# Kernel tuning notes

Measured on AMD Instinct MI355X. Metric: run time of the kernel, lower is better.

The kernel has to match this reference:

```python
import jax, jax.numpy as jnp
import numpy as np

NEG_BIAS = 1000000000.0


def setup_inputs() -> dict:
    key = jax.random.key(0)
    k1, k2 = jax.random.split(key)
    B, N, D = 8, 2048, 512
    inputs = jax.random.normal(k1, (B, N, D), dtype=jnp.float32)
    mask = jax.random.randint(k2, (B, N), 0, 2, dtype=jnp.int32)
    return {"inputs": inputs, "mask": mask}


def reference(inputs, mask):
    # inputs: [B, N, D], mask: [B, N]
    d = inputs.shape[-1]
    scale = 1.0 / jnp.sqrt(jnp.asarray(d, dtype=inputs.dtype))
    # e[b,i,j] = <x_i, x_j> / sqrt(d)
    e = jnp.einsum('bid,bjd->bij', inputs, inputs) * scale
    # K.expand_dims(mask) appends axis -1 -> [B, N, 1]; bias broadcasts over keys
    bias = (1.0 - mask.astype(inputs.dtype))[:, :, None] * NEG_BIAS
    e = e - bias
    a = jax.nn.softmax(e, axis=-1)  # [B, N, N]
    v = jnp.einsum('bij,bjd->bid', a, inputs)
    return v
```

## Files before the change

kernel.cpp:

```cpp
#include <hip/hip_runtime.h>

#define Bb 8
#define Nn 2048
#define Dd 512

#define KV 32
#define NT 64
#define SPS 40

#define KVF 64
#define NTF (Nn / KVF)
#define PPF 72

typedef __attribute__((ext_vector_type(8))) short bf8;
typedef __attribute__((ext_vector_type(4))) float f4;
typedef __attribute__((ext_vector_type(16))) float f16v;
struct __align__(16) U8 { unsigned short s[8]; };
struct __align__(8) US4 { unsigned short s[4]; };

__device__ __forceinline__ unsigned short f2bf(float f) {
  union { float f; unsigned u; } v; v.f = f;
  unsigned r = v.u + 0x7fffu + ((v.u >> 16) & 1u);
  return (unsigned short)(r >> 16);
}
__device__ __forceinline__ float bf2f(unsigned short h) {
  union { unsigned u; float f; } v; v.u = ((unsigned)h) << 16; return v.f;
}

__device__ __forceinline__ void gload_lds16(const unsigned short* g, unsigned short* l) {
  __builtin_amdgcn_global_load_lds(
      (const __attribute__((address_space(1))) void*)g,
      (__attribute__((address_space(3))) void*)l, 16, 0, 0);
}

__global__ __launch_bounds__(256)
void build_images(const float* __restrict__ X, unsigned short* __restrict__ W) {
  __shared__ float sT[KV * Dd];
  const int t = blockIdx.x, b = blockIdx.y, tid = threadIdx.x;
  const float* src = X + ((size_t)b * Nn + t * KV) * Dd;
#pragma unroll
  for (int i = 0; i < 16; ++i) {
    int idx = i * 256 + tid;
    *(float4*)(sT + idx * 4) = *(const float4*)(src + idx * 4);
  }
  __syncthreads();
  unsigned short* img = W + ((size_t)(b * NT + t) << 15);
#pragma unroll
  for (int i = 0; i < 8; ++i) {
    int slot = i * 256 + tid;
    int f = slot >> 6, L = slot & 63;
    const float* p = sT + (L & 31) * Dd + f * 16 + (L >> 5) * 8;
    U8 v;
#pragma unroll
    for (int e = 0; e < 8; ++e) v.s[e] = f2bf(p[e]);
    *(U8*)(img + slot * 8) = v;
  }
#pragma unroll
  for (int i = 0; i < 8; ++i) {
    int slot = i * 256 + tid;
    int fv = slot >> 6, L = slot & 63;
    int dcol = (fv >> 1) * 32 + (L & 31);
    int k0 = (fv & 1) * 16 + (L >> 5) * 8;
    U8 v;
#pragma unroll
    for (int e = 0; e < 8; ++e) v.s[e] = f2bf(sT[(k0 + e) * Dd + dcol]);
    *(U8*)(img + 16384 + slot * 8) = v;
  }
}

__global__ __launch_bounds__(512, 1)
void attn32(const unsigned short* __restrict__ W, const int* __restrict__ mask,
            float* __restrict__ out) {
  __shared__ unsigned short sBuf[2][32768];
  __shared__ unsigned short sSx[2 * 16 * 64 * 4];
  __shared__ unsigned short sP[2 * 32 * SPS];

  const int tid  = threadIdx.x;
  const int wave = tid >> 6;
  const int qg = wave >> 2, dq = wave & 3;
  const int lane = tid & 63;
  const int l31 = lane & 31, h = lane >> 5;
  const int rowsh = h * 4;
  const int bid = blockIdx.x;
  const int b = bid & 7;
  const int qb = bid >> 3;
  const int q0 = qb * 64;
  const int bN = b * NT;
  const float scale = 0.044194173824159216f;

  bf8 qf[8];
  {
    const unsigned short* qimg = W + ((size_t)(bN + qb * 2 + qg) << 15);
#pragma unroll
    for (int g = 0; g < 8; ++g)
      qf[g] = *(const bf8*)(qimg + (dq * 8 + g) * 512 + lane * 8);
  }

  float rs16[16];
  {
    int mv = mask[b * Nn + q0 + qg * 32 + l31];
    unsigned mb = (unsigned)(__ballot(mv != 0) & 0xffffffffull);
#pragma unroll
    for (int i = 0; i < 16; ++i) {
      int row = (i & 3) + 8 * (i >> 2) + rowsh;
      rs16[i] = ((mb >> row) & 1u) ? scale : 0.0f;
    }
  }

  bf8 ones;
#pragma unroll
  for (int i = 0; i < 8; ++i) ones[i] = (short)0x3F80;

  f16v o0, o1, o2, o3, lacc;
#pragma unroll
  for (int i = 0; i < 16; ++i) { o0[i] = 0.f; o1[i] = 0.f; o2[i] = 0.f; o3[i] = 0.f; lacc[i] = 0.f; }

  {
    const unsigned short* img0 = W + ((size_t)bN << 15);
#pragma unroll
    for (int i = 0; i < 8; ++i) {
      int chunk = i * 8 + wave;
      gload_lds16(img0 + chunk * 512 + lane * 8, sBuf[0] + chunk * 512);
    }
  }
  __syncthreads();

  int cur = 0;
  for (int t = 0; t < NT; ++t) {
    const unsigned short* sK = sBuf[cur];

    f16v sa, sb;
#pragma unroll
    for (int i = 0; i < 16; ++i) { sa[i] = 0.f; sb[i] = 0.f; }
#pragma unroll
    for (int g2 = 0; g2 < 4; ++g2) {
      bf8 k0 = *(const bf8*)(sK + (dq * 8 + g2 * 2) * 512 + lane * 8);
      bf8 k1 = *(const bf8*)(sK + (dq * 8 + g2 * 2 + 1) * 512 + lane * 8);
      sa = __builtin_amdgcn_mfma_f32_32x32x16_bf16(qf[g2 * 2], k0, sa, 0, 0, 0);
      sb = __builtin_amdgcn_mfma_f32_32x32x16_bf16(qf[g2 * 2 + 1], k1, sb, 0, 0, 0);
    }
#pragma unroll
    for (int i = 0; i < 16; ++i)
      sSx[((qg * 16 + i) * 64 + lane) * 4 + dq] = f2bf(sa[i] + sb[i]);
    __syncthreads();

    if (t + 1 < NT) {
      const unsigned short* gKn = W + ((size_t)(bN + t + 1) << 15);
      unsigned short* nb = sBuf[cur ^ 1];
#pragma unroll
      for (int i = 0; i < 8; ++i) {
        int chunk = i * 8 + wave;
        gload_lds16(gKn + chunk * 512 + lane * 8, nb + chunk * 512);
      }
    }

    unsigned short* Pq = sP + qg * 32 * SPS;
#pragma unroll
    for (int i = 0; i < 16; ++i) {
      US4 v = *(const US4*)(&sSx[((qg * 16 + i) * 64 + lane) * 4]);
      float e = (bf2f(v.s[0]) + bf2f(v.s[1]) + bf2f(v.s[2]) + bf2f(v.s[3])) * rs16[i];
      int row = (i & 3) + 8 * (i >> 2) + rowsh;
      Pq[row * SPS + l31] = f2bf(__expf(e));
    }
    bf8 af0 = *(const bf8*)(Pq + l31 * SPS + h * 8);
    bf8 af1 = *(const bf8*)(Pq + l31 * SPS + 16 + h * 8);

    lacc = __builtin_amdgcn_mfma_f32_32x32x16_bf16(af0, ones, lacc, 0, 0, 0);
    lacc = __builtin_amdgcn_mfma_f32_32x32x16_bf16(af1, ones, lacc, 0, 0, 0);

    const unsigned short* sV = sBuf[cur] + 16384;
    {
      bf8 v0 = *(const bf8*)(sV + ((dq * 4 + 0) * 2) * 512 + lane * 8);
      bf8 v1 = *(const bf8*)(sV + ((dq * 4 + 0) * 2 + 1) * 512 + lane * 8);
      o0 = __builtin_amdgcn_mfma_f32_32x32x16_bf16(af0, v0, o0, 0, 0, 0);
      o0 = __builtin_amdgcn_mfma_f32_32x32x16_bf16(af1, v1, o0, 0, 0, 0);
      v0 = *(const bf8*)(sV + ((dq * 4 + 1) * 2) * 512 + lane * 8);
      v1 = *(const bf8*)(sV + ((dq * 4 + 1) * 2 + 1) * 512 + lane * 8);
      o1 = __builtin_amdgcn_mfma_f32_32x32x16_bf16(af0, v0, o1, 0, 0, 0);
      o1 = __builtin_amdgcn_mfma_f32_32x32x16_bf16(af1, v1, o1, 0, 0, 0);
      v0 = *(const bf8*)(sV + ((dq * 4 + 2) * 2) * 512 + lane * 8);
      v1 = *(const bf8*)(sV + ((dq * 4 + 2) * 2 + 1) * 512 + lane * 8);
      o2 = __builtin_amdgcn_mfma_f32_32x32x16_bf16(af0, v0, o2, 0, 0, 0);
      o2 = __builtin_amdgcn_mfma_f32_32x32x16_bf16(af1, v1, o2, 0, 0, 0);
      v0 = *(const bf8*)(sV + ((dq * 4 + 3) * 2) * 512 + lane * 8);
      v1 = *(const bf8*)(sV + ((dq * 4 + 3) * 2 + 1) * 512 + lane * 8);
      o3 = __builtin_amdgcn_mfma_f32_32x32x16_bf16(af0, v0, o3, 0, 0, 0);
      o3 = __builtin_amdgcn_mfma_f32_32x32x16_bf16(af1, v1, o3, 0, 0, 0);
    }
    __syncthreads();
    cur ^= 1;
  }

#pragma unroll
  for (int i = 0; i < 16; ++i) {
    int row = (i & 3) + 8 * (i >> 2) + rowsh;
    size_t gr = (size_t)b * Nn + q0 + qg * 32 + row;
    float inv = 1.0f / lacc[i];
    out[gr * Dd + dq * 128 + 0 * 32 + l31] = o0[i] * inv;
    out[gr * Dd + dq * 128 + 1 * 32 + l31] = o1[i] * inv;
    out[gr * Dd + dq * 128 + 2 * 32 + l31] = o2[i] * inv;
    out[gr * Dd + dq * 128 + 3 * 32 + l31] = o3[i] * inv;
  }
}

__global__ __launch_bounds__(256, 1)
void attn_fb(const float* __restrict__ Xf, const int* __restrict__ mask,
             float* __restrict__ out) {
  __shared__ unsigned short sKf[KVF * Dd];
  __shared__ unsigned short sVt[Dd * KVF];
  __shared__ unsigned short sPf[4][16 * PPF];

  const int tid  = threadIdx.x;
  const int wave = tid >> 6, lane = tid & 63;
  const int lg = lane >> 4, ll = lane & 15;
  const int b  = blockIdx.y;
  const int q0 = blockIdx.x * 64 + wave * 16;

  bf8 qf[16];
  {
    const size_t qoff = ((size_t)b * Nn + q0 + ll) * Dd;
#pragma unroll
    for (int ch = 0; ch < 16; ++ch) {
      int doff = ch * 32 + lg * 8;
      float4 a = *(const float4*)(Xf + qoff + doff);
      float4 c = *(const float4*)(Xf + qoff + doff + 4);
      bf8 tt;
      tt[0] = (short)f2bf(a.x); tt[1] = (short)f2bf(a.y);
      tt[2] = (short)f2bf(a.z); tt[3] = (short)f2bf(a.w);
      tt[4] = (short)f2bf(c.x); tt[5] = (short)f2bf(c.y);
      tt[6] = (short)f2bf(c.z); tt[7] = (short)f2bf(c.w);
      qf[ch] = tt;
    }
  }
  float bias[4];
#pragma unroll
  for (int r = 0; r < 4; ++r)
    bias[r] = (1.0f - (float)mask[b * Nn + q0 + lg * 4 + r]) * 1e9f;
  float m[4], lsum[4];
  f4 o[32];
#pragma unroll
  for (int r = 0; r < 4; ++r) { m[r] = -1e30f; lsum[r] = 0.0f; }
#pragma unroll
  for (int ct = 0; ct < 32; ++ct) o[ct] = (f4){0.f, 0.f, 0.f, 0.f};
  const float scale = 0.044194173824159216f;

  for (int t = 0; t < NTF; ++t) {
    __syncthreads();
    const size_t base = ((size_t)b * Nn + t * KVF) * Dd;
#pragma unroll
    for (int it = 0; it < 16; ++it) {
      int idx = it * 256 + tid;
      int key = idx >> 6, c = idx & 63;
      const float* sp = Xf + base + key * Dd + c * 8;
      float4 a = *(const float4*)(sp);
      float4 d2 = *(const float4*)(sp + 4);
      U8 v;
      v.s[0] = f2bf(a.x); v.s[1] = f2bf(a.y); v.s[2] = f2bf(a.z); v.s[3] = f2bf(a.w);
      v.s[4] = f2bf(d2.x); v.s[5] = f2bf(d2.y); v.s[6] = f2bf(d2.z); v.s[7] = f2bf(d2.w);
      *(U8*)(sKf + key * 512 + ((c ^ (key & 7)) << 3)) = v;
      int ko = key >> 3, k7 = key & 7;
#pragma unroll
      for (int j = 0; j < 8; ++j) {
        int dd = c * 8 + j;
        sVt[dd * 64 + ((ko ^ j ^ (c & 7)) << 3) + k7] = v.s[j];
      }
    }
    __syncthreads();

    f4 s[4];
#pragma unroll
    for (int cc = 0; cc < 4; ++cc) s[cc] = (f4){0.f, 0.f, 0.f, 0.f};
#pragma unroll
    for (int ch = 0; ch < 16; ++ch)
#pragma unroll
      for (int cc = 0; cc < 4; ++cc) {
        int key = cc * 16 + ll;
        bf8 kf = *(const bf8*)(sKf + key * 512 + (((ch * 4 + lg) ^ (key & 7)) << 3));
        s[cc] = __builtin_amdgcn_mfma_f32_16x16x32_bf16(qf[ch], kf, s[cc], 0, 0, 0);
      }

    float e[4][4];
#pragma unroll
    for (int cc = 0; cc < 4; ++cc)
#pragma unroll
      for (int r = 0; r < 4; ++r) e[cc][r] = s[cc][r] * scale - bias[r];
    float tm[4];
#pragma unroll
    for (int r = 0; r < 4; ++r)
      tm[r] = fmaxf(fmaxf(e[0][r], e[1][r]), fmaxf(e[2][r], e[3][r]));
#pragma unroll
    for (int off = 1; off < 16; off <<= 1)
#pragma unroll
      for (int r = 0; r < 4; ++r) tm[r] = fmaxf(tm[r], __shfl_xor(tm[r], off));
    float mn[4]; bool change = false;
#pragma unroll
    for (int r = 0; r < 4; ++r) { mn[r] = fmaxf(m[r], tm[r]); change = change || (mn[r] > m[r]); }
    if (__any(change)) {
#pragma unroll
      for (int r = 0; r < 4; ++r) {
        float al = __expf(m[r] - mn[r]);
        lsum[r] *= al; m[r] = mn[r];
#pragma unroll
        for (int ct = 0; ct < 32; ++ct) o[ct][r] *= al;
      }
    }
    float ts[4] = {0.f, 0.f, 0.f, 0.f};
    unsigned short pb[4][4];
#pragma unroll
    for (int cc = 0; cc < 4; ++cc)
#pragma unroll
      for (int r = 0; r < 4; ++r) {
        float p = __expf(e[cc][r] - m[r]);
        ts[r] += p; pb[cc][r] = f2bf(p);
      }
#pragma unroll
    for (int off = 1; off < 16; off <<= 1)
#pragma unroll
      for (int r = 0; r < 4; ++r) ts[r] += __shfl_xor(ts[r], off);
#pragma unroll
    for (int r = 0; r < 4; ++r) lsum[r] += ts[r];

    unsigned short* Pw = sPf[wave];
#pragma unroll
    for (int cc = 0; cc < 4; ++cc)
#pragma unroll
      for (int r = 0; r < 4; ++r)
        Pw[(lg * 4 + r) * PPF + cc * 16 + ll] = pb[cc][r];
#pragma unroll
    for (int kc = 0; kc < 2; ++kc) {
      bf8 af = *(const bf8*)(Pw + ll * PPF + kc * 32 + lg * 8);
#pragma unroll
      for (int ct = 0; ct < 32; ++ct) {
        int d = ct * 16 + ll;
        bf8 vf = *(const bf8*)(sVt + d * 64 + (((kc * 4 + lg) ^ (d & 7) ^ ((d >> 3) & 7)) << 3));
        o[ct] = __builtin_amdgcn_mfma_f32_16x16x32_bf16(af, vf, o[ct], 0, 0, 0);
      }
    }
  }
  float inv[4];
#pragma unroll
  for (int r = 0; r < 4; ++r) inv[r] = 1.0f / lsum[r];
#pragma unroll
  for (int ct = 0; ct < 32; ++ct)
#pragma unroll
    for (int r = 0; r < 4; ++r) {
      size_t row = (size_t)b * Nn + q0 + lg * 4 + r;
      out[row * Dd + ct * 16 + ll] = o[ct][r] * inv[r];
    }
}

extern "C" void kernel_launch(void* const* d_in, const int* in_sizes, int n_in,
                              void* d_out, int out_size, void* d_ws, size_t ws_size,
                              hipStream_t stream) {
  (void)in_sizes; (void)n_in; (void)out_size;
  const float* X  = (const float*)d_in[0];
  const int* mask = (const int*)d_in[1];
  float* out = (float*)d_out;

  const size_t szImg = (size_t)Bb * NT * 65536;
  if (ws_size >= szImg) {
    unsigned short* W = (unsigned short*)d_ws;
    build_images<<<dim3(NT, Bb), 256, 0, stream>>>(X, W);
    attn32<<<256, 512, 0, stream>>>(W, mask, out);
  } else {
    attn_fb<<<dim3(Nn / 64, Bb), 256, 0, stream>>>(X, mask, out);
  }
}
```

Measured before the change: 153.8 us.

## Double key tile to 64 and read V fragments straight from global memory

Key/value tiles grow from 32 to 64 keys per iteration, which halves the loop trip count and the barriers per key. Waves are regrouped so that each pair splits the QK^T reduction over half the head dimension, and partial scores are exchanged through LDS. Only K is staged in LDS now, while V fragments are loaded directly from global/L2 inside the PV loop. The image builder converts to bf16 while loading from global memory. The risk is that the direct V global loads add latency to the inner loop, and that the extra barrier per iteration stalls the waves.

```diff
diff --git a/kernel.cpp b/kernel.cpp
--- a/kernel.cpp
+++ b/kernel.cpp
@@ -4,9 +4,9 @@
 #define Nn 2048
 #define Dd 512
 
-#define KV 32
-#define NT 64
-#define SPS 40
+#define KV2 64
+#define NT2 32
+#define SPS2 76
 
 #define KVF 64
 #define NTF (Nn / KVF)
@@ -35,75 +35,80 @@
 
 __global__ __launch_bounds__(256)
 void build_images(const float* __restrict__ X, unsigned short* __restrict__ W) {
-  __shared__ float sT[KV * Dd];
+  __shared__ unsigned short sT[KV2 * Dd];
   const int t = blockIdx.x, b = blockIdx.y, tid = threadIdx.x;
-  const float* src = X + ((size_t)b * Nn + t * KV) * Dd;
+  const float* src = X + ((size_t)b * Nn + t * KV2) * Dd;
+#pragma unroll
+  for (int i = 0; i < 32; ++i) {
+    int idx = i * 256 + tid;
+    float4 v = *(const float4*)(src + idx * 4);
+    US4 hx;
+    hx.s[0] = f2bf(v.x); hx.s[1] = f2bf(v.y);
+    hx.s[2] = f2bf(v.z); hx.s[3] = f2bf(v.w);
+    *(US4*)(sT + idx * 4) = hx;
+  }
+  __syncthreads();
+  unsigned short* img = W + ((size_t)(b * NT2 + t) << 16);
 #pragma unroll
   for (int i = 0; i < 16; ++i) {
-    int idx = i * 256 + tid;
-    *(float4*)(sT + idx * 4) = *(const float4*)(src + idx * 4);
-  }
-  __syncthreads();
-  unsigned short* img = W + ((size_t)(b * NT + t) << 15);
-#pragma unroll
-  for (int i = 0; i < 8; ++i) {
     int slot = i * 256 + tid;
-    int f = slot >> 6, L = slot & 63;
-    const float* p = sT + (L & 31) * Dd + f * 16 + (L >> 5) * 8;
-    U8 v;
-#pragma unroll
-    for (int e = 0; e < 8; ++e) v.s[e] = f2bf(p[e]);
+    int fk = slot >> 6, L = slot & 63;
+    int key = (fk >> 5) * 32 + (L & 31);
+    int d0 = (fk & 31) * 16 + (L >> 5) * 8;
+    U8 v = *(const U8*)(sT + key * Dd + d0);
     *(U8*)(img + slot * 8) = v;
   }
 #pragma unroll
-  for (int i = 0; i < 8; ++i) {
+  for (int i = 0; i < 16; ++i) {
     int slot = i * 256 + tid;
     int fv = slot >> 6, L = slot & 63;
-    int dcol = (fv >> 1) * 32 + (L & 31);
-    int k0 = (fv & 1) * 16 + (L >> 5) * 8;
+    int d = (fv >> 2) * 32 + (L & 31);
+    int k0 = (fv & 3) * 16 + (L >> 5) * 8;
     U8 v;
 #pragma unroll
-    for (int e = 0; e < 8; ++e) v.s[e] = f2bf(sT[(k0 + e) * Dd + dcol]);
-    *(U8*)(img + 16384 + slot * 8) = v;
+    for (int e = 0; e < 8; ++e) v.s[e] = sT[(k0 + e) * Dd + d];
+    *(U8*)(img + 32768 + slot * 8) = v;
   }
 }
 
 __global__ __launch_bounds__(512, 1)
-void attn32(const unsigned short* __restrict__ W, const int* __restrict__ mask,
+void attn64(const unsigned short* __restrict__ W, const int* __restrict__ mask,
             float* __restrict__ out) {
-  __shared__ unsigned short sBuf[2][32768];
-  __shared__ unsigned short sSx[2 * 16 * 64 * 4];
-  __shared__ unsigned short sP[2 * 32 * SPS];
+  __shared__ unsigned short sK[2][32768];
+  __shared__ unsigned short sSx[2][2][2][16][64];
+  __shared__ unsigned short sP[2][32][SPS2];
 
   const int tid  = threadIdx.x;
   const int wave = tid >> 6;
-  const int qg = wave >> 2, dq = wave & 3;
+  const int qg = wave >> 2;
+  const int kb = (wave >> 1) & 1;
+  const int dh = wave & 1;
+  const int dq = wave & 3;
   const int lane = tid & 63;
   const int l31 = lane & 31, h = lane >> 5;
-  const int rowsh = h * 4;
   const int bid = blockIdx.x;
   const int b = bid & 7;
   const int qb = bid >> 3;
-  const int q0 = qb * 64;
-  const int bN = b * NT;
+  const int bN = b * NT2;
   const float scale = 0.044194173824159216f;
 
-  bf8 qf[8];
+  bf8 qf[16];
   {
-    const unsigned short* qimg = W + ((size_t)(bN + qb * 2 + qg) << 15);
-#pragma unroll
-    for (int g = 0; g < 8; ++g)
-      qf[g] = *(const bf8*)(qimg + (dq * 8 + g) * 512 + lane * 8);
-  }
-
-  float rs16[16];
+    const unsigned short* qimg = W + ((size_t)(bN + qb) << 16);
+#pragma unroll
+    for (int j = 0; j < 16; ++j)
+      qf[j] = *(const bf8*)(qimg + ((qg * 32 + dh * 16 + j) * 64 + lane) * 8);
+  }
+
+  float rs8[8];
   {
-    int mv = mask[b * Nn + q0 + qg * 32 + l31];
+    int mv = mask[b * Nn + qb * 64 + qg * 32 + l31];
     unsigned mb = (unsigned)(__ballot(mv != 0) & 0xffffffffull);
 #pragma unroll
-    for (int i = 0; i < 16; ++i) {
-      int row = (i & 3) + 8 * (i >> 2) + rowsh;
-      rs16[i] = ((mb >> row) & 1u) ? scale : 0.0f;
+    for (int ii = 0; ii < 8; ++ii) {
+      int i = dh * 8 + ii;
+      int row = (i & 3) + 8 * (i >> 2) + 4 * h;
+      rs8[ii] = ((mb >> row) & 1u) ? scale : 0.0f;
     }
   }
 
@@ -116,37 +121,46 @@
   for (int i = 0; i < 16; ++i) { o0[i] = 0.f; o1[i] = 0.f; o2[i] = 0.f; o3[i] = 0.f; lacc[i] = 0.f; }
 
   {
-    const unsigned short* img0 = W + ((size_t)bN << 15);
+    const unsigned short* img0 = W + ((size_t)bN << 16);
 #pragma unroll
     for (int i = 0; i < 8; ++i) {
       int chunk = i * 8 + wave;
-      gload_lds16(img0 + chunk * 512 + lane * 8, sBuf[0] + chunk * 512);
+      gload_lds16(img0 + chunk * 512 + lane * 8, sK[0] + chunk * 512);
     }
   }
   __syncthreads();
 
   int cur = 0;
-  for (int t = 0; t < NT; ++t) {
-    const unsigned short* sK = sBuf[cur];
+  for (int t = 0; t < NT2; ++t) {
+    const unsigned short* sKc = sK[cur];
 
     f16v sa, sb;
 #pragma unroll
     for (int i = 0; i < 16; ++i) { sa[i] = 0.f; sb[i] = 0.f; }
 #pragma unroll
-    for (int g2 = 0; g2 < 4; ++g2) {
-      bf8 k0 = *(const bf8*)(sK + (dq * 8 + g2 * 2) * 512 + lane * 8);
-      bf8 k1 = *(const bf8*)(sK + (dq * 8 + g2 * 2 + 1) * 512 + lane * 8);
-      sa = __builtin_amdgcn_mfma_f32_32x32x16_bf16(qf[g2 * 2], k0, sa, 0, 0, 0);
-      sb = __builtin_amdgcn_mfma_f32_32x32x16_bf16(qf[g2 * 2 + 1], k1, sb, 0, 0, 0);
+    for (int j2 = 0; j2 < 8; ++j2) {
+      bf8 k0 = *(const bf8*)(sKc + ((kb * 32 + dh * 16 + j2 * 2) * 64 + lane) * 8);
+      bf8 k1 = *(const bf8*)(sKc + ((kb * 32 + dh * 16 + j2 * 2 + 1) * 64 + lane) * 8);
+      sa = __builtin_amdgcn_mfma_f32_32x32x16_bf16(qf[j2 * 2], k0, sa, 0, 0, 0);
+      sb = __builtin_amdgcn_mfma_f32_32x32x16_bf16(qf[j2 * 2 + 1], k1, sb, 0, 0, 0);
     }
 #pragma unroll
     for (int i = 0; i < 16; ++i)
-      sSx[((qg * 16 + i) * 64 + lane) * 4 + dq] = f2bf(sa[i] + sb[i]);
-    __syncthreads();
-
-    if (t + 1 < NT) {
-      const unsigned short* gKn = W + ((size_t)(bN + t + 1) << 15);
-      unsigned short* nb = sBuf[cur ^ 1];
+      sSx[qg][kb][dh][i][lane] = f2bf(sa[i] + sb[i]);
+    __syncthreads();
+
+#pragma unroll
+    for (int ii = 0; ii < 8; ++ii) {
+      int i = dh * 8 + ii;
+      float e = (sa[i] + sb[i] + bf2f(sSx[qg][kb][dh ^ 1][i][lane])) * rs8[ii];
+      int row = (i & 3) + 8 * (i >> 2) + 4 * h;
+      sP[qg][row][kb * 32 + l31] = f2bf(__expf(e));
+    }
+    __syncthreads();
+
+    if (t + 1 < NT2) {
+      const unsigned short* gKn = W + ((size_t)(bN + t + 1) << 16);
+      unsigned short* nb = sK[cur ^ 1];
 #pragma unroll
       for (int i = 0; i < 8; ++i) {
         int chunk = i * 8 + wave;
@@ -154,38 +168,25 @@
       }
     }
 
-    unsigned short* Pq = sP + qg * 32 * SPS;
-#pragma unroll
-    for (int i = 0; i < 16; ++i) {
-      US4 v = *(const US4*)(&sSx[((qg * 16 + i) * 64 + lane) * 4]);
-      float e = (bf2f(v.s[0]) + bf2f(v.s[1]) + bf2f(v.s[2]) + bf2f(v.s[3])) * rs16[i];
-      int row = (i & 3) + 8 * (i >> 2) + rowsh;
-      Pq[row * SPS + l31] = f2bf(__expf(e));
-    }
-    bf8 af0 = *(const bf8*)(Pq + l31 * SPS + h * 8);
-    bf8 af1 = *(const bf8*)(Pq + l31 * SPS + 16 + h * 8);
-
-    lacc = __builtin_amdgcn_mfma_f32_32x32x16_bf16(af0, ones, lacc, 0, 0, 0);
-    lacc = __builtin_amdgcn_mfma_f32_32x32x16_bf16(af1, ones, lacc, 0, 0, 0);
-
-    const unsigned short* sV = sBuf[cur] + 16384;
-    {
-      bf8 v0 = *(const bf8*)(sV + ((dq * 4 + 0) * 2) * 512 + lane * 8);
-      bf8 v1 = *(const bf8*)(sV + ((dq * 4 + 0) * 2 + 1) * 512 + lane * 8);
-      o0 = __builtin_amdgcn_mfma_f32_32x32x16_bf16(af0, v0, o0, 0, 0, 0);
-      o0 = __builtin_amdgcn_mfma_f32_32x32x16_bf16(af1, v1, o0, 0, 0, 0);
-      v0 = *(const bf8*)(sV + ((dq * 4 + 1) * 2) * 512 + lane * 8);
-      v1 = *(const bf8*)(sV + ((dq * 4 + 1) * 2 + 1) * 512 + lane * 8);
-      o1 = __builtin_amdgcn_mfma_f32_32x32x16_bf16(af0, v0, o1, 0, 0, 0);
-      o1 = __builtin_amdgcn_mfma_f32_32x32x16_bf16(af1, v1, o1, 0, 0, 0);
-      v0 = *(const bf8*)(sV + ((dq * 4 + 2) * 2) * 512 + lane * 8);
-      v1 = *(const bf8*)(sV + ((dq * 4 + 2) * 2 + 1) * 512 + lane * 8);
-      o2 = __builtin_amdgcn_mfma_f32_32x32x16_bf16(af0, v0, o2, 0, 0, 0);
-      o2 = __builtin_amdgcn_mfma_f32_32x32x16_bf16(af1, v1, o2, 0, 0, 0);
-      v0 = *(const bf8*)(sV + ((dq * 4 + 3) * 2) * 512 + lane * 8);
-      v1 = *(const bf8*)(sV + ((dq * 4 + 3) * 2 + 1) * 512 + lane * 8);
-      o3 = __builtin_amdgcn_mfma_f32_32x32x16_bf16(af0, v0, o3, 0, 0, 0);
-      o3 = __builtin_amdgcn_mfma_f32_32x32x16_bf16(af1, v1, o3, 0, 0, 0);
+    bf8 af[4];
+#pragma unroll
+    for (int m = 0; m < 4; ++m)
+      af[m] = *(const bf8*)(&sP[qg][l31][m * 16 + h * 8]);
+#pragma unroll
+    for (int m = 0; m < 4; ++m)
+      lacc = __builtin_amdgcn_mfma_f32_32x32x16_bf16(af[m], ones, lacc, 0, 0, 0);
+
+    const unsigned short* gV = W + ((size_t)(bN + t) << 16) + 32768;
+#pragma unroll
+    for (int m = 0; m < 4; ++m) {
+      bf8 v0 = *(const bf8*)(gV + (((dq * 4 + 0) * 4 + m) * 64 + lane) * 8);
+      bf8 v1 = *(const bf8*)(gV + (((dq * 4 + 1) * 4 + m) * 64 + lane) * 8);
+      bf8 v2 = *(const bf8*)(gV + (((dq * 4 + 2) * 4 + m) * 64 + lane) * 8);
+      bf8 v3 = *(const bf8*)(gV + (((dq * 4 + 3) * 4 + m) * 64 + lane) * 8);
+      o0 = __builtin_amdgcn_mfma_f32_32x32x16_bf16(af[m], v0, o0, 0, 0, 0);
+      o1 = __builtin_amdgcn_mfma_f32_32x32x16_bf16(af[m], v1, o1, 0, 0, 0);
+      o2 = __builtin_amdgcn_mfma_f32_32x32x16_bf16(af[m], v2, o2, 0, 0, 0);
+      o3 = __builtin_amdgcn_mfma_f32_32x32x16_bf16(af[m], v3, o3, 0, 0, 0);
     }
     __syncthreads();
     cur ^= 1;
@@ -193,8 +194,8 @@
 
 #pragma unroll
   for (int i = 0; i < 16; ++i) {
-    int row = (i & 3) + 8 * (i >> 2) + rowsh;
-    size_t gr = (size_t)b * Nn + q0 + qg * 32 + row;
+    int row = (i & 3) + 8 * (i >> 2) + 4 * h;
+    size_t gr = (size_t)b * Nn + qb * 64 + qg * 32 + row;
     float inv = 1.0f / lacc[i];
     out[gr * Dd + dq * 128 + 0 * 32 + l31] = o0[i] * inv;
     out[gr * Dd + dq * 128 + 1 * 32 + l31] = o1[i] * inv;
@@ -357,11 +358,11 @@
   const int* mask = (const int*)d_in[1];
   float* out = (float*)d_out;
 
-  const size_t szImg = (size_t)Bb * NT * 65536;
+  const size_t szImg = (size_t)Bb * NT2 * 131072;
   if (ws_size >= szImg) {
     unsigned short* W = (unsigned short*)d_ws;
-    build_images<<<dim3(NT, Bb), 256, 0, stream>>>(X, W);
-    attn32<<<256, 512, 0, stream>>>(W, mask, out);
+    build_images<<<dim3(NT2, Bb), 256, 0, stream>>>(X, W);
+    attn64<<<256, 512, 0, stream>>>(W, mask, out);
   } else {
     attn_fb<<<dim3(Nn / 64, Bb), 256, 0, stream>>>(X, mask, out);
   }
```

After: 174.5 us. 13.4% more time.
